# Optimization experiments

Hardware: AMD Instinct MI355X
Metric: run time of the kernel (lower is better)

Reference implementation:

```python
import jax, jax.numpy as jnp
import numpy as np

B = 1024          # batch
H = 1024          # rnn_num_hidden
T = 512           # max_length (encoder timesteps)
NUM = 44          # numeric features
EMB = [(30490, 64), (7, 8), (12, 8), (3, 4)]
IN = NUM + sum(d for _, d in EMB)   # input_size = 128


def lstm_cell(x, h, c, w_ih, w_hh, b_ih, b_hh):
    # PyTorch LSTM gate order: i, f, g, o
    g = x @ w_ih.T + h @ w_hh.T + b_ih + b_hh
    i, f, gg, o = jnp.split(g, 4, axis=-1)
    c2 = jax.nn.sigmoid(f) * c + jax.nn.sigmoid(i) * jnp.tanh(gg)
    h2 = jax.nn.sigmoid(o) * jnp.tanh(c2)
    return h2, c2


def setup_inputs():
    key = jax.random.key(0)
    ks = iter(jax.random.split(key, 32))
    nrm = lambda shape, s=0.02: (s * jax.random.normal(next(ks), shape)).astype(jnp.float32)
    return {
        "x": nrm((B, 1, NUM), 1.0),
        "x_emb": jax.random.randint(next(ks), (B, 1, 4), 0, 3),
        "h0": nrm((2, B, H), 1.0),
        "c0": nrm((2, B, H), 1.0),
        "encoder_outputs": nrm((T, B, H), 1.0),
        "emb0": nrm(EMB[0]), "emb1": nrm(EMB[1]), "emb2": nrm(EMB[2]), "emb3": nrm(EMB[3]),
        "attn_w": nrm((T, IN + 2 * H)), "attn_b": nrm((T,)),
        "comb_w": nrm((IN, IN + H)), "comb_b": nrm((IN,)),
        "w_ih0": nrm((4 * H, IN)), "w_hh0": nrm((4 * H, H)),
        "b_ih0": nrm((4 * H,)), "b_hh0": nrm((4 * H,)),
        "w_ih1": nrm((4 * H, H)), "w_hh1": nrm((4 * H, H)),
        "b_ih1": nrm((4 * H,)), "b_hh1": nrm((4 * H,)),
        "pred_w": nrm((1, H)), "pred_b": nrm((1,)),
    }


def reference(x, x_emb, h0, c0, encoder_outputs, emb0, emb1, emb2, emb3,
              attn_w, attn_b, comb_w, comb_b,
              w_ih0, w_hh0, b_ih0, b_hh0, w_ih1, w_hh1, b_ih1, b_hh1,
              pred_w, pred_b):
    xt = x.transpose(1, 0, 2)[0]                       # (B, NUM)
    ids = x_emb.transpose(1, 0, 2)[0]                  # (B, 4)
    e = jnp.concatenate([emb0[ids[:, 0]], emb1[ids[:, 1]],
                         emb2[ids[:, 2]], emb3[ids[:, 3]]], axis=1)
    x_rnn = jnp.concatenate([xt, e], axis=1)           # (B, IN)
    attn_in = jnp.concatenate([x_rnn, h0[0], c0[0]], axis=1)       # (B, IN+2H)
    aw = jax.nn.softmax(attn_in @ attn_w.T + attn_b, axis=1)       # (B, T)
    ctx = jnp.einsum('bt,tbh->bh', aw, encoder_outputs)            # (B, H)
    comb = jnp.concatenate([x_rnn, ctx], axis=1) @ comb_w.T + comb_b  # (B, IN)
    h1, c1 = lstm_cell(comb, h0[0], c0[0], w_ih0, w_hh0, b_ih0, b_hh0)
    h2, c2 = lstm_cell(h1, h0[1], c0[1], w_ih1, w_hh1, b_ih1, b_hh1)
    out = h2 @ pred_w.T + pred_b                       # (B, 1)
    return out, (jnp.stack([h1, h2]), jnp.stack([c1, c2])), aw
```

## Files before the change

kernel.cpp:

```cpp
#include <hip/hip_runtime.h>
#include <hip/hip_bf16.h>

#define B 1024
#define H 1024
#define T 512
#define NUM 44
#define IN 128
#define AK (IN + 2 * H)
#define XC (IN + H)
#define G4 (4 * H)

typedef __attribute__((ext_vector_type(8))) short s16x8;
typedef __attribute__((ext_vector_type(4))) float f32x4;

__device__ __forceinline__ unsigned short f2bf(float f) {
    unsigned u = __float_as_uint(f);
    unsigned r = (u + 0x7fffu + ((u >> 16) & 1u)) >> 16;
    return (unsigned short)r;
}

__device__ __forceinline__ void gload16(const ushort* g, ushort* l) {
    __builtin_amdgcn_global_load_lds(
        (const __attribute__((address_space(1))) void*)g,
        (__attribute__((address_space(3))) void*)l,
        16, 0, 0);
}

#define TM 128
#define TN 128
#define TK 32

__device__ __forceinline__ void gemm_core(
    const ushort* __restrict__ X, const ushort* __restrict__ W,
    const float* __restrict__ bias1, const float* __restrict__ bias2,
    const float* __restrict__ Cin, float* __restrict__ Cf, ushort* __restrict__ Cb,
    int kbeg, int kend, int ldx, int ldw, int ldc,
    int m0, int n0, ushort (*As)[TK], ushort (*Bs)[TK])
{
    const int tid = threadIdx.x;
    const int lane = tid & 63;
    const int wid = tid >> 6;
    const int wm = wid >> 1, wn = wid & 1;
    const int srow = wid * 32 + (lane >> 2);
    const int skc  = (lane & 3) * 8;

    f32x4 acc[4][4] = {};

    for (int k0 = kbeg; k0 < kend; k0 += TK) {
        gload16(X + (size_t)(m0 + srow) * ldx + k0 + skc,      &As[wid * 32][0]);
        gload16(X + (size_t)(m0 + srow + 16) * ldx + k0 + skc, &As[wid * 32 + 16][0]);
        gload16(W + (size_t)(n0 + srow) * ldw + k0 + skc,      &Bs[wid * 32][0]);
        gload16(W + (size_t)(n0 + srow + 16) * ldw + k0 + skc, &Bs[wid * 32 + 16][0]);
        __syncthreads();

        s16x8 a[4], b[4];
        #pragma unroll
        for (int m = 0; m < 4; ++m)
            a[m] = *(const s16x8*)&As[wm * 64 + m * 16 + (lane & 15)][(lane >> 4) * 8];
        #pragma unroll
        for (int n = 0; n < 4; ++n)
            b[n] = *(const s16x8*)&Bs[wn * 64 + n * 16 + (lane & 15)][(lane >> 4) * 8];
        #pragma unroll
        for (int m = 0; m < 4; ++m)
            #pragma unroll
            for (int n = 0; n < 4; ++n)
                acc[m][n] = __builtin_amdgcn_mfma_f32_16x16x32_bf16(a[m], b[n], acc[m][n], 0, 0, 0);
        __syncthreads();
    }

    #pragma unroll
    for (int m = 0; m < 4; ++m) {
        #pragma unroll
        for (int n = 0; n < 4; ++n) {
            int col = n0 + wn * 64 + n * 16 + (lane & 15);
            float badd = (bias1 ? bias1[col] : 0.f) + (bias2 ? bias2[col] : 0.f);
            #pragma unroll
            for (int j = 0; j < 4; ++j) {
                int row = m0 + wm * 64 + m * 16 + (lane >> 4) * 4 + j;
                float v = acc[m][n][j] + badd;
                if (Cin) v += Cin[(size_t)row * ldc + col];
                if (Cf) Cf[(size_t)row * ldc + col] = v;
                if (Cb) Cb[(size_t)row * ldc + col] = f2bf(v);
            }
        }
    }
}

__global__ __launch_bounds__(256) void gemm_kernel(
    const ushort* __restrict__ X, const ushort* __restrict__ W,
    const float* __restrict__ bias1, const float* __restrict__ bias2,
    const float* __restrict__ Cin, float* __restrict__ Cf, ushort* __restrict__ Cb,
    int Kchunk, int ldx, int ldw, int ldc, size_t Czstride)
{
    __shared__ ushort As[TM][TK];
    __shared__ ushort Bs[TN][TK];
    int kbeg = blockIdx.z * Kchunk;
    gemm_core(X, W, bias1, bias2, Cin,
              Cf ? Cf + (size_t)blockIdx.z * Czstride : nullptr, Cb,
              kbeg, kbeg + Kchunk, ldx, ldw, ldc,
              blockIdx.y * TM, blockIdx.x * TN, As, Bs);
}

#define CN0 524288
#define CN1 278528
#define CN2 131072
#define CN3 1048576
#define CN4 1048576
#define CN5 1048576
#define CNT (CN0+CN1+CN2+CN3+CN4+CN5)

__global__ __launch_bounds__(256) void convert_all_kernel(
    const float* __restrict__ s0, const float* __restrict__ s1, const float* __restrict__ s2,
    const float* __restrict__ s3, const float* __restrict__ s4, const float* __restrict__ s5,
    ushort* __restrict__ d0, ushort* __restrict__ d1, ushort* __restrict__ d2,
    ushort* __restrict__ d3, ushort* __restrict__ d4, ushort* __restrict__ d5)
{
    int i = blockIdx.x * 256 + threadIdx.x;
    const float* s; ushort* d;
    if (i < CN0) { s = s0; d = d0; }
    else if ((i -= CN0) < CN1) { s = s1; d = d1; }
    else if ((i -= CN1) < CN2) { s = s2; d = d2; }
    else if ((i -= CN2) < CN3) { s = s3; d = d3; }
    else if ((i -= CN3) < CN4) { s = s4; d = d4; }
    else if ((i -= CN4) < CN5) { s = s5; d = d5; }
    else return;
    float4 v = ((const float4*)s)[i];
    ushort4 o;
    o.x = f2bf(v.x); o.y = f2bf(v.y); o.z = f2bf(v.z); o.w = f2bf(v.w);
    ((ushort4*)d)[i] = o;
}

__global__ __launch_bounds__(256) void transpose_combw_kernel(
    const float* __restrict__ comb_w, ushort* __restrict__ outT)
{
    int idx = blockIdx.x * 256 + threadIdx.x;
    int j = idx >> 7;
    int k = idx & 127;
    outT[idx] = f2bf(comb_w[(size_t)k * XC + j]);
}

__global__ __launch_bounds__(256) void bias_f_kernel(
    const float* __restrict__ w_ih0, const float* __restrict__ comb_b,
    const float* __restrict__ b_ih0, const float* __restrict__ b_hh0,
    float* __restrict__ biasf)
{
    __shared__ float cb[IN];
    int i = blockIdx.x * 256 + threadIdx.x;
    for (int j = threadIdx.x; j < IN; j += 256) cb[j] = comb_b[j];
    __syncthreads();
    float s = b_ih0[i] + b_hh0[i];
    const float* row = w_ih0 + (size_t)i * IN;
    #pragma unroll 8
    for (int j = 0; j < IN; ++j) s += row[j] * cb[j];
    biasf[i] = s;
}

__global__ __launch_bounds__(256) void build_attn_in_kernel(
    const float* __restrict__ x, const int* __restrict__ x_emb,
    const float* __restrict__ h0, const float* __restrict__ c0,
    const float* __restrict__ e0, const float* __restrict__ e1,
    const float* __restrict__ e2, const float* __restrict__ e3,
    ushort* __restrict__ attn_in, ushort* __restrict__ xctx)
{
    int b = blockIdx.x;
    int id0 = x_emb[b * 4 + 0];
    int id1 = x_emb[b * 4 + 1];
    int id2 = x_emb[b * 4 + 2];
    int id3 = x_emb[b * 4 + 3];
    ushort* dst = attn_in + (size_t)b * AK;
    for (int j = threadIdx.x; j < AK; j += 256) {
        float v;
        if (j < 44)        v = x[b * NUM + j];
        else if (j < 108)  v = e0[id0 * 64 + (j - 44)];
        else if (j < 116)  v = e1[id1 * 8 + (j - 108)];
        else if (j < 124)  v = e2[id2 * 8 + (j - 116)];
        else if (j < 128)  v = e3[id3 * 4 + (j - 124)];
        else if (j < 1152) v = h0[b * H + (j - 128)];
        else               v = c0[b * H + (j - 1152)];
        unsigned short bf = f2bf(v);
        dst[j] = bf;
        if (j < IN) xctx[(size_t)b * XC + j] = bf;
    }
}

__global__ __launch_bounds__(256) void mega_kernel(
    const ushort* __restrict__ h0_bf, const ushort* __restrict__ whh0_bf,
    const ushort* __restrict__ whh1_bf, float* __restrict__ g1buf, float* __restrict__ g2buf,
    const ushort* __restrict__ wih0_bf, const ushort* __restrict__ comb_wT_bf,
    ushort* __restrict__ W_f_bf,
    const float* __restrict__ logits_part, const float* __restrict__ attn_b,
    float* __restrict__ aw_out, const float* __restrict__ enc, ushort* __restrict__ xctx)
{
    __shared__ union {
        struct { ushort As[TM][TK]; ushort Bs[TN][TK]; } g;
        struct { float w[T]; float red[8]; } c;
    } sh;

    const int bid = blockIdx.x;
    const int gid_before = (int)(((long)bid * 800) / 1824);
    const int gid_after  = (int)(((long)(bid + 1) * 800) / 1824);
    const bool is_gemm = gid_after > gid_before;

    if (is_gemm) {
        const int rid = gid_before;
        if (rid < 512) {
            int layer = rid >> 8;
            int t = rid & 255;
            int m0 = (t >> 5) * TM;
            int n0 = (t & 31) * TN;
            gemm_core(h0_bf + (size_t)layer * B * H, layer ? whh1_bf : whh0_bf,
                      nullptr, nullptr, nullptr, layer ? g2buf : g1buf, nullptr,
                      0, H, H, H, G4, m0, n0, sh.g.As, sh.g.Bs);
        } else {
            int t = rid - 512;
            int m0 = (t / 9) * TM;
            int n0 = (t % 9) * TN;
            gemm_core(wih0_bf, comb_wT_bf, nullptr, nullptr, nullptr, nullptr, W_f_bf,
                      0, IN, IN, IN, XC, m0, n0, sh.g.As, sh.g.Bs);
        }
    } else {
        int b = bid - gid_before;
        int tid = threadIdx.x;
        float v0 = attn_b[tid], v1 = attn_b[tid + 256];
        #pragma unroll
        for (int z = 0; z < 4; ++z) {
            const float* lp = logits_part + (size_t)z * B * T + (size_t)b * T;
            v0 += lp[tid];
            v1 += lp[tid + 256];
        }
        float m = fmaxf(v0, v1);
        #pragma unroll
        for (int off = 32; off > 0; off >>= 1) m = fmaxf(m, __shfl_down(m, off, 64));
        if ((tid & 63) == 0) sh.c.red[tid >> 6] = m;
        __syncthreads();
        m = fmaxf(fmaxf(sh.c.red[0], sh.c.red[1]), fmaxf(sh.c.red[2], sh.c.red[3]));
        float e0 = expf(v0 - m), e1 = expf(v1 - m);
        float s = e0 + e1;
        #pragma unroll
        for (int off = 32; off > 0; off >>= 1) s += __shfl_down(s, off, 64);
        if ((tid & 63) == 0) sh.c.red[4 + (tid >> 6)] = s;
        __syncthreads();
        s = sh.c.red[4] + sh.c.red[5] + sh.c.red[6] + sh.c.red[7];
        float inv = 1.0f / s;
        float w0 = e0 * inv, w1 = e1 * inv;
        sh.c.w[tid] = w0;
        sh.c.w[tid + 256] = w1;
        aw_out[(size_t)b * T + tid]       = w0;
        aw_out[(size_t)b * T + tid + 256] = w1;
        __syncthreads();

        int h0i = tid * 4;
        const float* p = enc + (size_t)b * H + h0i;
        float4 acc = {0.f, 0.f, 0.f, 0.f};
        #pragma unroll 8
        for (int t = 0; t < T; ++t) {
            float4 v = *(const float4*)(p + (size_t)t * B * H);
            float sw = sh.c.w[t];
            acc.x += sw * v.x; acc.y += sw * v.y; acc.z += sw * v.z; acc.w += sw * v.w;
        }
        ushort4 o;
        o.x = f2bf(acc.x); o.y = f2bf(acc.y); o.z = f2bf(acc.z); o.w = f2bf(acc.w);
        *(ushort4*)(xctx + (size_t)b * XC + IN + h0i) = o;
    }
}

__device__ __forceinline__ float sigmf(float v) { return 1.0f / (1.0f + expf(-v)); }

__global__ __launch_bounds__(256) void lstm_pointwise_kernel(
    const float* __restrict__ g, const float* __restrict__ c_in,
    float* __restrict__ h_out, float* __restrict__ c_out,
    ushort* __restrict__ h_bf)
{
    int idx = blockIdx.x * 256 + threadIdx.x;
    int b = idx >> 10;
    int j = idx & 1023;
    const float* gr = g + (size_t)b * G4;
    float gi = gr[j];
    float gf = gr[j + H];
    float gc = gr[j + 2 * H];
    float go = gr[j + 3 * H];
    float c = sigmf(gf) * c_in[idx] + sigmf(gi) * tanhf(gc);
    float h = sigmf(go) * tanhf(c);
    h_out[idx] = h;
    c_out[idx] = c;
    if (h_bf) h_bf[idx] = f2bf(h);
}

__global__ __launch_bounds__(256) void pred_kernel(
    const float* __restrict__ h2, const float* __restrict__ pw,
    const float* __restrict__ pb, float* __restrict__ out)
{
    int b = blockIdx.x;
    const float* row = h2 + (size_t)b * H;
    float s = 0.f;
    for (int j = threadIdx.x; j < H; j += 256) s += row[j] * pw[j];
    #pragma unroll
    for (int off = 32; off > 0; off >>= 1) s += __shfl_down(s, off, 64);
    __shared__ float sm[4];
    if ((threadIdx.x & 63) == 0) sm[threadIdx.x >> 6] = s;
    __syncthreads();
    if (threadIdx.x == 0) out[b] = sm[0] + sm[1] + sm[2] + sm[3] + pb[0];
}

extern "C" void kernel_launch(void* const* d_in, const int* in_sizes, int n_in,
                              void* d_out, int out_size, void* d_ws, size_t ws_size,
                              hipStream_t stream) {
    (void)in_sizes; (void)n_in; (void)out_size; (void)ws_size;
    const float* x      = (const float*)d_in[0];
    const int*   x_emb  = (const int*)d_in[1];
    const float* h0     = (const float*)d_in[2];
    const float* c0     = (const float*)d_in[3];
    const float* enc    = (const float*)d_in[4];
    const float* emb0   = (const float*)d_in[5];
    const float* emb1   = (const float*)d_in[6];
    const float* emb2   = (const float*)d_in[7];
    const float* emb3   = (const float*)d_in[8];
    const float* attn_w = (const float*)d_in[9];
    const float* attn_b = (const float*)d_in[10];
    const float* comb_w = (const float*)d_in[11];
    const float* comb_b = (const float*)d_in[12];
    const float* w_ih0  = (const float*)d_in[13];
    const float* w_hh0  = (const float*)d_in[14];
    const float* b_ih0  = (const float*)d_in[15];
    const float* b_hh0  = (const float*)d_in[16];
    const float* w_ih1  = (const float*)d_in[17];
    const float* w_hh1  = (const float*)d_in[18];
    const float* b_ih1  = (const float*)d_in[19];
    const float* b_hh1  = (const float*)d_in[20];
    const float* pred_w = (const float*)d_in[21];
    const float* pred_b = (const float*)d_in[22];

    float* out = (float*)d_out;
    const size_t BH = (size_t)B * H;
    float* h1_out = out + 1024;
    float* h2_out = out + 1024 + BH;
    float* c1_out = out + 1024 + 2 * BH;
    float* c2_out = out + 1024 + 3 * BH;
    float* aw_out = out + 1024 + 4 * BH;

    char* w = (char*)d_ws;
    ushort* attn_in_bf = (ushort*)w;  w += (size_t)B * AK * 2;
    ushort* h0_bf      = (ushort*)w;  w += (size_t)2 * BH * 2;
    ushort* attn_w_bf  = (ushort*)w;  w += (size_t)T * AK * 2;
    ushort* wih0_bf    = (ushort*)w;  w += (size_t)G4 * IN * 2;
    ushort* whh0_bf    = (ushort*)w;  w += (size_t)G4 * H * 2;
    ushort* wih1_bf    = (ushort*)w;  w += (size_t)G4 * H * 2;
    ushort* whh1_bf    = (ushort*)w;  w += (size_t)G4 * H * 2;
    ushort* comb_wT_bf = (ushort*)w;  w += (size_t)XC * IN * 2;
    ushort* W_f_bf     = (ushort*)w;  w += (size_t)G4 * XC * 2;
    float*  bias_f     = (float*)w;   w += (size_t)G4 * 4;
    ushort* xctx_bf    = (ushort*)w;  w += (size_t)B * XC * 2;
    ushort* h1_bf      = (ushort*)w;  w += (size_t)BH * 2;
    float*  logits_p   = (float*)w;   w += (size_t)4 * B * T * 4;
    float*  g1buf      = (float*)w;   w += (size_t)B * G4 * 4;
    float*  g2buf      = (float*)w;   w += (size_t)B * G4 * 4;

    convert_all_kernel<<<(CNT + 255) / 256, 256, 0, stream>>>(
        h0, attn_w, w_ih0, w_hh0, w_ih1, w_hh1,
        h0_bf, attn_w_bf, wih0_bf, whh0_bf, wih1_bf, whh1_bf);

    transpose_combw_kernel<<<(XC * IN) / 256, 256, 0, stream>>>(comb_w, comb_wT_bf);

    bias_f_kernel<<<G4 / 256, 256, 0, stream>>>(w_ih0, comb_b, b_ih0, b_hh0, bias_f);

    build_attn_in_kernel<<<B, 256, 0, stream>>>(x, x_emb, h0, c0, emb0, emb1, emb2, emb3,
                                                attn_in_bf, xctx_bf);

    gemm_kernel<<<dim3(T / TN, B / TM, 4), 256, 0, stream>>>(
        attn_in_bf, attn_w_bf, nullptr, nullptr, nullptr, logits_p, nullptr,
        544, AK, AK, T, (size_t)B * T);

    mega_kernel<<<1824, 256, 0, stream>>>(
        h0_bf, whh0_bf, whh1_bf, g1buf, g2buf,
        wih0_bf, comb_wT_bf, W_f_bf,
        logits_p, attn_b, aw_out, enc, xctx_bf);

    gemm_kernel<<<dim3(G4 / TN, B / TM, 1), 256, 0, stream>>>(
        xctx_bf, W_f_bf, bias_f, nullptr, g1buf, g1buf, nullptr,
        XC, XC, XC, G4, 0);

    lstm_pointwise_kernel<<<(B * H) / 256, 256, 0, stream>>>(g1buf, c0, h1_out, c1_out, h1_bf);

    gemm_kernel<<<dim3(G4 / TN, B / TM, 1), 256, 0, stream>>>(
        h1_bf, wih1_bf, b_ih1, b_hh1, g2buf, g2buf, nullptr,
        H, H, H, G4, 0);

    lstm_pointwise_kernel<<<(B * H) / 256, 256, 0, stream>>>(g2buf, c0 + BH, h2_out, c2_out, nullptr);

    pred_kernel<<<1024, 256, 0, stream>>>(h2_out, pred_w, pred_b, out);
}
```

Baseline: 661.9 us.

## Restructure pipeline: merged preamble, all-GEMM launch, split-T context, 64-row GEMM tiles

Merges the conversion, transpose, bias and input-building kernels into one preamble launch. All GEMMs that need no context (attention logits, both hidden-state GEMMs, the folded weight GEMM) now share one launch, replacing the mega-kernel that overlapped them with the context reduction. The context reduction over 512 timesteps is split into two halves per batch row, giving 2048 blocks with 16-deep batched loads, followed by a small reduce kernel. The two large LSTM input GEMMs use 64x128 tiles to double the block count. Serialising the context pass after the GEMMs removes the earlier overlap, and the partial-context buffer reuses the start of the workspace that held inputs already consumed.

```diff
diff --git a/kernel.cpp b/kernel.cpp
--- a/kernel.cpp
+++ b/kernel.cpp
@@ -9,6 +9,7 @@
 #define AK (IN + 2 * H)
 #define XC (IN + H)
 #define G4 (4 * H)
+#define BH ((size_t)B * H)
 
 typedef __attribute__((ext_vector_type(8))) short s16x8;
 typedef __attribute__((ext_vector_type(4))) float f32x4;
@@ -86,182 +87,239 @@
     }
 }
 
-__global__ __launch_bounds__(256) void gemm_kernel(
+__global__ __launch_bounds__(256) void allgemms_kernel(
+    const ushort* __restrict__ attn_in, const ushort* __restrict__ attn_w_bf,
+    float* __restrict__ logits_p,
+    const ushort* __restrict__ h0_bf,
+    const ushort* __restrict__ whh0_bf, const ushort* __restrict__ whh1_bf,
+    float* __restrict__ g1buf, float* __restrict__ g2buf,
+    const ushort* __restrict__ wih0_bf, const ushort* __restrict__ comb_wT_bf,
+    ushort* __restrict__ W_f_bf)
+{
+    __shared__ ushort As[TM][TK];
+    __shared__ ushort Bs[TN][TK];
+    const int rid = blockIdx.x;
+    if (rid < 128) {
+        int z = rid >> 5, t = rid & 31;
+        int m0 = (t >> 2) * TM, n0 = (t & 3) * TN;
+        gemm_core(attn_in, attn_w_bf, nullptr, nullptr, nullptr,
+                  logits_p + (size_t)z * B * T, nullptr,
+                  z * 544, z * 544 + 544, AK, AK, T, m0, n0, As, Bs);
+    } else if (rid < 640) {
+        int layer = (rid - 128) >> 8;
+        int t = (rid - 128) & 255;
+        int m0 = (t >> 5) * TM, n0 = (t & 31) * TN;
+        gemm_core(h0_bf + (size_t)layer * BH, layer ? whh1_bf : whh0_bf,
+                  nullptr, nullptr, nullptr, layer ? g2buf : g1buf, nullptr,
+                  0, H, H, H, G4, m0, n0, As, Bs);
+    } else {
+        int t = rid - 640;
+        int m0 = (t / 9) * TM, n0 = (t % 9) * TN;
+        gemm_core(wih0_bf, comb_wT_bf, nullptr, nullptr, nullptr, nullptr, W_f_bf,
+                  0, IN, IN, IN, XC, m0, n0, As, Bs);
+    }
+}
+
+__global__ __launch_bounds__(256) void gemm64_kernel(
     const ushort* __restrict__ X, const ushort* __restrict__ W,
     const float* __restrict__ bias1, const float* __restrict__ bias2,
-    const float* __restrict__ Cin, float* __restrict__ Cf, ushort* __restrict__ Cb,
-    int Kchunk, int ldx, int ldw, int ldc, size_t Czstride)
-{
-    __shared__ ushort As[TM][TK];
-    __shared__ ushort Bs[TN][TK];
-    int kbeg = blockIdx.z * Kchunk;
-    gemm_core(X, W, bias1, bias2, Cin,
-              Cf ? Cf + (size_t)blockIdx.z * Czstride : nullptr, Cb,
-              kbeg, kbeg + Kchunk, ldx, ldw, ldc,
-              blockIdx.y * TM, blockIdx.x * TN, As, Bs);
-}
-
-#define CN0 524288
-#define CN1 278528
-#define CN2 131072
-#define CN3 1048576
-#define CN4 1048576
-#define CN5 1048576
-#define CNT (CN0+CN1+CN2+CN3+CN4+CN5)
-
-__global__ __launch_bounds__(256) void convert_all_kernel(
-    const float* __restrict__ s0, const float* __restrict__ s1, const float* __restrict__ s2,
-    const float* __restrict__ s3, const float* __restrict__ s4, const float* __restrict__ s5,
-    ushort* __restrict__ d0, ushort* __restrict__ d1, ushort* __restrict__ d2,
-    ushort* __restrict__ d3, ushort* __restrict__ d4, ushort* __restrict__ d5)
-{
-    int i = blockIdx.x * 256 + threadIdx.x;
-    const float* s; ushort* d;
-    if (i < CN0) { s = s0; d = d0; }
-    else if ((i -= CN0) < CN1) { s = s1; d = d1; }
-    else if ((i -= CN1) < CN2) { s = s2; d = d2; }
-    else if ((i -= CN2) < CN3) { s = s3; d = d3; }
-    else if ((i -= CN3) < CN4) { s = s4; d = d4; }
-    else if ((i -= CN4) < CN5) { s = s5; d = d5; }
-    else return;
-    float4 v = ((const float4*)s)[i];
-    ushort4 o;
-    o.x = f2bf(v.x); o.y = f2bf(v.y); o.z = f2bf(v.z); o.w = f2bf(v.w);
-    ((ushort4*)d)[i] = o;
-}
-
-__global__ __launch_bounds__(256) void transpose_combw_kernel(
-    const float* __restrict__ comb_w, ushort* __restrict__ outT)
-{
-    int idx = blockIdx.x * 256 + threadIdx.x;
-    int j = idx >> 7;
-    int k = idx & 127;
-    outT[idx] = f2bf(comb_w[(size_t)k * XC + j]);
-}
-
-__global__ __launch_bounds__(256) void bias_f_kernel(
-    const float* __restrict__ w_ih0, const float* __restrict__ comb_b,
+    const float* __restrict__ Cin, float* __restrict__ Cf,
+    int K, int ldx, int ldw, int ldc)
+{
+    __shared__ ushort As[64][TK];
+    __shared__ ushort Bs[128][TK];
+    const int tid = threadIdx.x;
+    const int lane = tid & 63;
+    const int wid = tid >> 6;
+    const int wm = wid >> 1, wn = wid & 1;
+    const int m0 = blockIdx.y * 64;
+    const int n0 = blockIdx.x * 128;
+    const int skc = (lane & 3) * 8;
+
+    f32x4 acc[2][4] = {};
+
+    for (int k0 = 0; k0 < K; k0 += TK) {
+        gload16(X + (size_t)(m0 + wid * 16 + (lane >> 2)) * ldx + k0 + skc, &As[wid * 16][0]);
+        gload16(W + (size_t)(n0 + wid * 32 + (lane >> 2)) * ldw + k0 + skc, &Bs[wid * 32][0]);
+        gload16(W + (size_t)(n0 + wid * 32 + 16 + (lane >> 2)) * ldw + k0 + skc, &Bs[wid * 32 + 16][0]);
+        __syncthreads();
+        s16x8 a[2], b[4];
+        #pragma unroll
+        for (int m = 0; m < 2; ++m)
+            a[m] = *(const s16x8*)&As[wm * 32 + m * 16 + (lane & 15)][(lane >> 4) * 8];
+        #pragma unroll
+        for (int n = 0; n < 4; ++n)
+            b[n] = *(const s16x8*)&Bs[wn * 64 + n * 16 + (lane & 15)][(lane >> 4) * 8];
+        #pragma unroll
+        for (int m = 0; m < 2; ++m)
+            #pragma unroll
+            for (int n = 0; n < 4; ++n)
+                acc[m][n] = __builtin_amdgcn_mfma_f32_16x16x32_bf16(a[m], b[n], acc[m][n], 0, 0, 0);
+        __syncthreads();
+    }
+
+    #pragma unroll
+    for (int m = 0; m < 2; ++m) {
+        #pragma unroll
+        for (int n = 0; n < 4; ++n) {
+            int col = n0 + wn * 64 + n * 16 + (lane & 15);
+            float badd = (bias1 ? bias1[col] : 0.f) + (bias2 ? bias2[col] : 0.f);
+            #pragma unroll
+            for (int j = 0; j < 4; ++j) {
+                int row = m0 + wm * 32 + m * 16 + (lane >> 4) * 4 + j;
+                float v = acc[m][n][j] + badd;
+                if (Cin) v += Cin[(size_t)row * ldc + col];
+                Cf[(size_t)row * ldc + col] = v;
+            }
+        }
+    }
+}
+
+#define P0 2048
+#define P1 (P0 + 1088)
+#define P2 (P1 + 512)
+#define P3 (P2 + 4096)
+#define P4 (P3 + 4096)
+#define P5 (P4 + 4096)
+#define P6 (P5 + 576)
+#define P7 (P6 + 16)
+#define P8 (P7 + 1024)
+
+__global__ __launch_bounds__(256) void preamble_kernel(
+    const float* __restrict__ h0, const float* __restrict__ attn_w,
+    const float* __restrict__ w_ih0, const float* __restrict__ w_hh0,
+    const float* __restrict__ w_ih1, const float* __restrict__ w_hh1,
+    const float* __restrict__ comb_w, const float* __restrict__ comb_b,
     const float* __restrict__ b_ih0, const float* __restrict__ b_hh0,
-    float* __restrict__ biasf)
-{
-    __shared__ float cb[IN];
-    int i = blockIdx.x * 256 + threadIdx.x;
-    for (int j = threadIdx.x; j < IN; j += 256) cb[j] = comb_b[j];
-    __syncthreads();
-    float s = b_ih0[i] + b_hh0[i];
-    const float* row = w_ih0 + (size_t)i * IN;
-    #pragma unroll 8
-    for (int j = 0; j < IN; ++j) s += row[j] * cb[j];
-    biasf[i] = s;
-}
-
-__global__ __launch_bounds__(256) void build_attn_in_kernel(
     const float* __restrict__ x, const int* __restrict__ x_emb,
-    const float* __restrict__ h0, const float* __restrict__ c0,
+    const float* __restrict__ c0,
     const float* __restrict__ e0, const float* __restrict__ e1,
     const float* __restrict__ e2, const float* __restrict__ e3,
+    ushort* __restrict__ h0_bf, ushort* __restrict__ attn_w_bf,
+    ushort* __restrict__ wih0_bf, ushort* __restrict__ whh0_bf,
+    ushort* __restrict__ wih1_bf, ushort* __restrict__ whh1_bf,
+    ushort* __restrict__ comb_wT, float* __restrict__ biasf,
     ushort* __restrict__ attn_in, ushort* __restrict__ xctx)
 {
-    int b = blockIdx.x;
-    int id0 = x_emb[b * 4 + 0];
-    int id1 = x_emb[b * 4 + 1];
-    int id2 = x_emb[b * 4 + 2];
-    int id3 = x_emb[b * 4 + 3];
-    ushort* dst = attn_in + (size_t)b * AK;
-    for (int j = threadIdx.x; j < AK; j += 256) {
-        float v;
-        if (j < 44)        v = x[b * NUM + j];
-        else if (j < 108)  v = e0[id0 * 64 + (j - 44)];
-        else if (j < 116)  v = e1[id1 * 8 + (j - 108)];
-        else if (j < 124)  v = e2[id2 * 8 + (j - 116)];
-        else if (j < 128)  v = e3[id3 * 4 + (j - 124)];
-        else if (j < 1152) v = h0[b * H + (j - 128)];
-        else               v = c0[b * H + (j - 1152)];
-        unsigned short bf = f2bf(v);
-        dst[j] = bf;
-        if (j < IN) xctx[(size_t)b * XC + j] = bf;
-    }
-}
-
-__global__ __launch_bounds__(256) void mega_kernel(
-    const ushort* __restrict__ h0_bf, const ushort* __restrict__ whh0_bf,
-    const ushort* __restrict__ whh1_bf, float* __restrict__ g1buf, float* __restrict__ g2buf,
-    const ushort* __restrict__ wih0_bf, const ushort* __restrict__ comb_wT_bf,
-    ushort* __restrict__ W_f_bf,
-    const float* __restrict__ logits_part, const float* __restrict__ attn_b,
-    float* __restrict__ aw_out, const float* __restrict__ enc, ushort* __restrict__ xctx)
-{
-    __shared__ union {
-        struct { ushort As[TM][TK]; ushort Bs[TN][TK]; } g;
-        struct { float w[T]; float red[8]; } c;
-    } sh;
-
     const int bid = blockIdx.x;
-    const int gid_before = (int)(((long)bid * 800) / 1824);
-    const int gid_after  = (int)(((long)(bid + 1) * 800) / 1824);
-    const bool is_gemm = gid_after > gid_before;
-
-    if (is_gemm) {
-        const int rid = gid_before;
-        if (rid < 512) {
-            int layer = rid >> 8;
-            int t = rid & 255;
-            int m0 = (t >> 5) * TM;
-            int n0 = (t & 31) * TN;
-            gemm_core(h0_bf + (size_t)layer * B * H, layer ? whh1_bf : whh0_bf,
-                      nullptr, nullptr, nullptr, layer ? g2buf : g1buf, nullptr,
-                      0, H, H, H, G4, m0, n0, sh.g.As, sh.g.Bs);
-        } else {
-            int t = rid - 512;
-            int m0 = (t / 9) * TM;
-            int n0 = (t % 9) * TN;
-            gemm_core(wih0_bf, comb_wT_bf, nullptr, nullptr, nullptr, nullptr, W_f_bf,
-                      0, IN, IN, IN, XC, m0, n0, sh.g.As, sh.g.Bs);
+    const int tid = threadIdx.x;
+
+    if (bid < P5) {
+        const float* s; ushort* d; int f;
+        if (bid < P0)      { f = bid * 256 + tid;        s = h0;     d = h0_bf; }
+        else if (bid < P1) { f = (bid - P0) * 256 + tid; s = attn_w; d = attn_w_bf; }
+        else if (bid < P2) { f = (bid - P1) * 256 + tid; s = w_ih0;  d = wih0_bf; }
+        else if (bid < P3) { f = (bid - P2) * 256 + tid; s = w_hh0;  d = whh0_bf; }
+        else if (bid < P4) { f = (bid - P3) * 256 + tid; s = w_ih1;  d = wih1_bf; }
+        else               { f = (bid - P4) * 256 + tid; s = w_hh1;  d = whh1_bf; }
+        float4 v = ((const float4*)s)[f];
+        ushort4 o = {f2bf(v.x), f2bf(v.y), f2bf(v.z), f2bf(v.w)};
+        ((ushort4*)d)[f] = o;
+    } else if (bid < P6) {
+        int e = (bid - P5) * 256 + tid;
+        int j = e >> 7, k = e & 127;
+        comb_wT[e] = f2bf(comb_w[(size_t)k * XC + j]);
+    } else if (bid < P7) {
+        __shared__ float cb[IN];
+        for (int i = tid; i < IN; i += 256) cb[i] = comb_b[i];
+        __syncthreads();
+        int i = (bid - P6) * 256 + tid;
+        float s = b_ih0[i] + b_hh0[i];
+        const float* row = w_ih0 + (size_t)i * IN;
+        #pragma unroll 8
+        for (int j = 0; j < IN; ++j) s += row[j] * cb[j];
+        biasf[i] = s;
+    } else {
+        int b = bid - P7;
+        int id0 = x_emb[b * 4 + 0];
+        int id1 = x_emb[b * 4 + 1];
+        int id2 = x_emb[b * 4 + 2];
+        int id3 = x_emb[b * 4 + 3];
+        ushort* dst = attn_in + (size_t)b * AK;
+        for (int j = tid; j < AK; j += 256) {
+            float v;
+            if (j < 44)        v = x[b * NUM + j];
+            else if (j < 108)  v = e0[id0 * 64 + (j - 44)];
+            else if (j < 116)  v = e1[id1 * 8 + (j - 108)];
+            else if (j < 124)  v = e2[id2 * 8 + (j - 116)];
+            else if (j < 128)  v = e3[id3 * 4 + (j - 124)];
+            else if (j < 1152) v = h0[b * H + (j - 128)];
+            else               v = c0[b * H + (j - 1152)];
+            unsigned short bf = f2bf(v);
+            dst[j] = bf;
+            if (j < IN) xctx[(size_t)b * XC + j] = bf;
         }
-    } else {
-        int b = bid - gid_before;
-        int tid = threadIdx.x;
-        float v0 = attn_b[tid], v1 = attn_b[tid + 256];
-        #pragma unroll
-        for (int z = 0; z < 4; ++z) {
-            const float* lp = logits_part + (size_t)z * B * T + (size_t)b * T;
-            v0 += lp[tid];
-            v1 += lp[tid + 256];
-        }
-        float m = fmaxf(v0, v1);
-        #pragma unroll
-        for (int off = 32; off > 0; off >>= 1) m = fmaxf(m, __shfl_down(m, off, 64));
-        if ((tid & 63) == 0) sh.c.red[tid >> 6] = m;
-        __syncthreads();
-        m = fmaxf(fmaxf(sh.c.red[0], sh.c.red[1]), fmaxf(sh.c.red[2], sh.c.red[3]));
-        float e0 = expf(v0 - m), e1 = expf(v1 - m);
-        float s = e0 + e1;
-        #pragma unroll
-        for (int off = 32; off > 0; off >>= 1) s += __shfl_down(s, off, 64);
-        if ((tid & 63) == 0) sh.c.red[4 + (tid >> 6)] = s;
-        __syncthreads();
-        s = sh.c.red[4] + sh.c.red[5] + sh.c.red[6] + sh.c.red[7];
-        float inv = 1.0f / s;
-        float w0 = e0 * inv, w1 = e1 * inv;
-        sh.c.w[tid] = w0;
-        sh.c.w[tid + 256] = w1;
+    }
+}
+
+__global__ __launch_bounds__(256) void ctx_kernel(
+    const float* __restrict__ enc, const float* __restrict__ logits_p,
+    const float* __restrict__ attn_b, float* __restrict__ aw_out,
+    float* __restrict__ ctxp)
+{
+    const int b = blockIdx.x >> 1;
+    const int z = blockIdx.x & 1;
+    const int tid = threadIdx.x;
+    __shared__ float w[T];
+    __shared__ float red[8];
+
+    float v0 = attn_b[tid], v1 = attn_b[tid + 256];
+    #pragma unroll
+    for (int q = 0; q < 4; ++q) {
+        const float* lp = logits_p + (size_t)q * B * T + (size_t)b * T;
+        v0 += lp[tid];
+        v1 += lp[tid + 256];
+    }
+    float m = fmaxf(v0, v1);
+    #pragma unroll
+    for (int off = 32; off > 0; off >>= 1) m = fmaxf(m, __shfl_down(m, off, 64));
+    if ((tid & 63) == 0) red[tid >> 6] = m;
+    __syncthreads();
+    m = fmaxf(fmaxf(red[0], red[1]), fmaxf(red[2], red[3]));
+    float e0 = expf(v0 - m), e1 = expf(v1 - m);
+    float s = e0 + e1;
+    #pragma unroll
+    for (int off = 32; off > 0; off >>= 1) s += __shfl_down(s, off, 64);
+    if ((tid & 63) == 0) red[4 + (tid >> 6)] = s;
+    __syncthreads();
+    s = red[4] + red[5] + red[6] + red[7];
+    float inv = 1.0f / s;
+    float w0 = e0 * inv, w1 = e1 * inv;
+    w[tid] = w0;
+    w[tid + 256] = w1;
+    if (z == 0) {
         aw_out[(size_t)b * T + tid]       = w0;
         aw_out[(size_t)b * T + tid + 256] = w1;
-        __syncthreads();
-
-        int h0i = tid * 4;
-        const float* p = enc + (size_t)b * H + h0i;
-        float4 acc = {0.f, 0.f, 0.f, 0.f};
-        #pragma unroll 8
-        for (int t = 0; t < T; ++t) {
-            float4 v = *(const float4*)(p + (size_t)t * B * H);
-            float sw = sh.c.w[t];
-            acc.x += sw * v.x; acc.y += sw * v.y; acc.z += sw * v.z; acc.w += sw * v.w;
+    }
+    __syncthreads();
+
+    const float* p = enc + (size_t)(z * 256) * B * H + (size_t)b * H + tid * 4;
+    float4 acc = {0.f, 0.f, 0.f, 0.f};
+    for (int t0 = 0; t0 < 256; t0 += 16) {
+        float4 vv[16];
+        #pragma unroll
+        for (int u = 0; u < 16; ++u)
+            vv[u] = *(const float4*)(p + (size_t)(t0 + u) * B * H);
+        #pragma unroll
+        for (int u = 0; u < 16; ++u) {
+            float sw = w[z * 256 + t0 + u];
+            acc.x += sw * vv[u].x; acc.y += sw * vv[u].y;
+            acc.z += sw * vv[u].z; acc.w += sw * vv[u].w;
         }
-        ushort4 o;
-        o.x = f2bf(acc.x); o.y = f2bf(acc.y); o.z = f2bf(acc.z); o.w = f2bf(acc.w);
-        *(ushort4*)(xctx + (size_t)b * XC + IN + h0i) = o;
-    }
+    }
+    *(float4*)(ctxp + (size_t)z * BH + (size_t)b * H + tid * 4) = acc;
+}
+
+__global__ __launch_bounds__(256) void ctx_reduce_kernel(
+    const float* __restrict__ ctxp, ushort* __restrict__ xctx)
+{
+    int i = blockIdx.x * 256 + threadIdx.x;
+    float4 a = ((const float4*)ctxp)[i];
+    float4 c = ((const float4*)(ctxp + BH))[i];
+    int f = i * 4;
+    int b = f >> 10, h = f & 1023;
+    ushort4 o = {f2bf(a.x + c.x), f2bf(a.y + c.y), f2bf(a.z + c.z), f2bf(a.w + c.w)};
+    *(ushort4*)(xctx + (size_t)b * XC + IN + h) = o;
 }
 
 __device__ __forceinline__ float sigmf(float v) { return 1.0f / (1.0f + expf(-v)); }
@@ -331,7 +389,6 @@
     const float* pred_b = (const float*)d_in[22];
 
     float* out = (float*)d_out;
-    const size_t BH = (size_t)B * H;
     float* h1_out = out + 1024;
     float* h2_out = out + 1024 + BH;
     float* c1_out = out + 1024 + 2 * BH;
@@ -354,38 +411,32 @@
     float*  logits_p   = (float*)w;   w += (size_t)4 * B * T * 4;
     float*  g1buf      = (float*)w;   w += (size_t)B * G4 * 4;
     float*  g2buf      = (float*)w;   w += (size_t)B * G4 * 4;
-
-    convert_all_kernel<<<(CNT + 255) / 256, 256, 0, stream>>>(
-        h0, attn_w, w_ih0, w_hh0, w_ih1, w_hh1,
-        h0_bf, attn_w_bf, wih0_bf, whh0_bf, wih1_bf, whh1_bf);
-
-    transpose_combw_kernel<<<(XC * IN) / 256, 256, 0, stream>>>(comb_w, comb_wT_bf);
-
-    bias_f_kernel<<<G4 / 256, 256, 0, stream>>>(w_ih0, comb_b, b_ih0, b_hh0, bias_f);
-
-    build_attn_in_kernel<<<B, 256, 0, stream>>>(x, x_emb, h0, c0, emb0, emb1, emb2, emb3,
-                                                attn_in_bf, xctx_bf);
-
-    gemm_kernel<<<dim3(T / TN, B / TM, 4), 256, 0, stream>>>(
-        attn_in_bf, attn_w_bf, nullptr, nullptr, nullptr, logits_p, nullptr,
-        544, AK, AK, T, (size_t)B * T);
-
-    mega_kernel<<<1824, 256, 0, stream>>>(
+    float*  ctxp       = (float*)d_ws;
+
+    preamble_kernel<<<P8, 256, 0, stream>>>(
+        h0, attn_w, w_ih0, w_hh0, w_ih1, w_hh1, comb_w, comb_b, b_ih0, b_hh0,
+        x, x_emb, c0, emb0, emb1, emb2, emb3,
+        h0_bf, attn_w_bf, wih0_bf, whh0_bf, wih1_bf, whh1_bf, comb_wT_bf, bias_f,
+        attn_in_bf, xctx_bf);
+
+    allgemms_kernel<<<928, 256, 0, stream>>>(
+        attn_in_bf, attn_w_bf, logits_p,
         h0_bf, whh0_bf, whh1_bf, g1buf, g2buf,
-        wih0_bf, comb_wT_bf, W_f_bf,
-        logits_p, attn_b, aw_out, enc, xctx_bf);
-
-    gemm_kernel<<<dim3(G4 / TN, B / TM, 1), 256, 0, stream>>>(
-        xctx_bf, W_f_bf, bias_f, nullptr, g1buf, g1buf, nullptr,
-        XC, XC, XC, G4, 0);
-
-    lstm_pointwise_kernel<<<(B * H) / 256, 256, 0, stream>>>(g1buf, c0, h1_out, c1_out, h1_bf);
-
-    gemm_kernel<<<dim3(G4 / TN, B / TM, 1), 256, 0, stream>>>(
-        h1_bf, wih1_bf, b_ih1, b_hh1, g2buf, g2buf, nullptr,
-        H, H, H, G4, 0);
-
-    lstm_pointwise_kernel<<<(B * H) / 256, 256, 0, stream>>>(g2buf, c0 + BH, h2_out, c2_out, nullptr);
+        wih0_bf, comb_wT_bf, W_f_bf);
+
+    ctx_kernel<<<2048, 256, 0, stream>>>(enc, logits_p, attn_b, aw_out, ctxp);
+
+    ctx_reduce_kernel<<<(int)(BH / 4 / 256), 256, 0, stream>>>(ctxp, xctx_bf);
+
+    gemm64_kernel<<<dim3(G4 / 128, B / 64), 256, 0, stream>>>(
+        xctx_bf, W_f_bf, bias_f, nullptr, g1buf, g1buf, XC, XC, XC, G4);
+
+    lstm_pointwise_kernel<<<(int)(BH / 256), 256, 0, stream>>>(g1buf, c0, h1_out, c1_out, h1_bf);
+
+    gemm64_kernel<<<dim3(G4 / 128, B / 64), 256, 0, stream>>>(
+        h1_bf, wih1_bf, b_ih1, b_hh1, g2buf, g2buf, H, H, H, G4);
+
+    lstm_pointwise_kernel<<<(int)(BH / 256), 256, 0, stream>>>(g2buf, c0 + BH, h2_out, c2_out, nullptr);
 
     pred_kernel<<<1024, 256, 0, stream>>>(h2_out, pred_w, pred_b, out);
 }
```

Result: faster. 609.6 us (-7.9%).
